# Kernel tuning notes

Measured on AMD Instinct MI355X. Metric: run time of the kernel, lower is better.

The kernel has to match this reference:

```python
import jax, jax.numpy as jnp
import numpy as np

NUM_HEADS = 8
D_MODEL = 512
D_K = D_MODEL // NUM_HEADS


def setup_inputs() -> dict:
    key = jax.random.key(0)
    ks = jax.random.split(key, 16)
    B, L, Dq = 4, 2048, 512
    s = 1.0 / np.sqrt(D_MODEL)
    inp = {
        "query": jax.random.normal(ks[0], (B, L, Dq), jnp.float32),
        "key": jax.random.normal(ks[1], (B, L, Dq), jnp.float32),
        "value": jax.random.normal(ks[2], (B, L, Dq), jnp.float32),
        "mask": jax.random.randint(ks[3], (B, L), 0, 2, jnp.int32),
        "Wq": jax.random.normal(ks[4], (Dq, D_MODEL), jnp.float32) * s,
        "bq": jax.random.normal(ks[5], (D_MODEL,), jnp.float32) * s,
        "Wk": jax.random.normal(ks[6], (Dq, D_MODEL), jnp.float32) * s,
        "bk": jax.random.normal(ks[7], (D_MODEL,), jnp.float32) * s,
        "Wv": jax.random.normal(ks[8], (Dq, D_MODEL), jnp.float32) * s,
        "bv": jax.random.normal(ks[9], (D_MODEL,), jnp.float32) * s,
        "Wo": jax.random.normal(ks[10], (D_MODEL, D_MODEL), jnp.float32) * s,
        "bo": jax.random.normal(ks[11], (D_MODEL,), jnp.float32) * s,
    }
    return inp


def _mha(query, key, value, mask, Wq, bq, Wk, bk, Wv, bv, Wo, bo):
    B, Q, _ = query.shape
    KV = key.shape[1]
    # projections, split into heads: (B, H, L, d_k)
    q = (query @ Wq + bq).reshape(B, Q, NUM_HEADS, D_K).transpose(0, 2, 1, 3)
    k = (key @ Wk + bk).reshape(B, KV, NUM_HEADS, D_K).transpose(0, 2, 1, 3)
    v = (value @ Wv + bv).reshape(B, KV, NUM_HEADS, D_K).transpose(0, 2, 1, 3)
    # full (B, H, Q, KV) score matrix, as in the original module
    scores = jnp.einsum("bhqd,bhkd->bhqk", q, k) / jnp.sqrt(jnp.asarray(D_K, q.dtype))
    m = (mask == 0)[:, None, None, :]  # (B,1,1,KV) broadcasting like unsqueeze(1)
    min_val = jnp.finfo(scores.dtype).min
    scores = jnp.where(m, min_val, scores)
    attn = jax.nn.softmax(scores, axis=-1)
    attn = jnp.where(m, 0.0, attn)
    xs = jnp.einsum("bhqk,bhkd->bhqd", attn, v)
    xs = xs.transpose(0, 2, 1, 3).reshape(B, Q, NUM_HEADS * D_K)
    return xs @ Wo + bo


def reference(query, key, value, mask, Wq, bq, Wk, bk, Wv, bv, Wo, bo):
    return _mha(query, key, value, mask, Wq, bq, Wk, bk, Wv, bv, Wo, bo)
```

## Files before the change

### kernel.cpp

```cpp
#include <hip/hip_runtime.h>
#include <math.h>

#define Bq 4
#define Lq 2048
#define NH 8
#define LDP6 36

typedef __attribute__((ext_vector_type(8))) __bf16 bf16x8;
typedef __attribute__((ext_vector_type(4))) float f32x4;
#define MFMA16(a,b,c) __builtin_amdgcn_mfma_f32_16x16x32_bf16(a,b,c,0,0,0)

__device__ __forceinline__ void async16(const void* g, void* l) {
    __builtin_amdgcn_global_load_lds(
        (const __attribute__((address_space(1))) unsigned int*)g,
        (__attribute__((address_space(3))) unsigned int*)l, 16, 0, 0);
}

__device__ __forceinline__ void splitbf(float x, ushort& h, ushort& l) {
    unsigned u = __float_as_uint(x);
    h = (ushort)(u >> 16);
    float hf = __uint_as_float(u & 0xffff0000u);
    l = (ushort)(__float_as_uint(x - hf) >> 16);
}
__device__ __forceinline__ ushort rnebf(float x) {
    unsigned u = __float_as_uint(x);
    return (ushort)((u + 0x7fffu + ((u >> 16) & 1u)) >> 16);
}

__global__ __launch_bounds__(256) void maskscan_kernel(
    const int* __restrict__ mask, int* __restrict__ idx, int* __restrict__ nvalid)
{
    __shared__ int ss[256];
    const int b = blockIdx.x, tid = threadIdx.x;
    int m[8], s = 0;
    #pragma unroll
    for (int j = 0; j < 8; ++j) { m[j] = (mask[b * 2048 + tid * 8 + j] != 0); s += m[j]; }
    int v = s;
    ss[tid] = v;
    __syncthreads();
    for (int off = 1; off < 256; off <<= 1) {
        int t_ = (tid >= off) ? ss[tid - off] : 0;
        __syncthreads();
        v += t_;
        ss[tid] = v;
        __syncthreads();
    }
    int pos = v - s;
    #pragma unroll
    for (int j = 0; j < 8; ++j) if (m[j]) idx[b * 2048 + pos++] = tid * 8 + j;
    int tot = ss[255];
    if (tid == 0) nvalid[b] = tot;
    for (int k = tot + tid; k < 2048; k += 256) idx[b * 2048 + k] = 0;
}

__global__ __launch_bounds__(256) void xrne3_kernel(
    const float* __restrict__ X0, const float* __restrict__ X1, const float* __restrict__ X2,
    const int* __restrict__ idx, const int* __restrict__ nvalid,
    ushort* __restrict__ Xr)
{
    const int z = blockIdx.z;
    const float* X = (z == 0) ? X0 : (z == 1) ? X1 : X2;
    const size_t ebase = (size_t)blockIdx.x * 2048 + (size_t)threadIdx.x * 8;
    const int row = (int)(ebase >> 9), col = (int)(ebase & 511);
    const int b = row >> 11, r = row & 2047;
    if (z >= 1) {
        int nv = nvalid[b];
        int nvpad = ((nv + 127) >> 7) << 7;
        if (r >= nvpad) return;
    }
    const int srow = (z == 0) ? row : (b * 2048 + idx[b * 2048 + r]);
    const float* src = X + (size_t)srow * 512 + col;
    float4 a = *(const float4*)(src);
    float4 bb = *(const float4*)(src + 4);
    float vv[8] = {a.x, a.y, a.z, a.w, bb.x, bb.y, bb.z, bb.w};
    ushort hs[8];
    #pragma unroll
    for (int j = 0; j < 8; ++j) hs[j] = rnebf(vv[j]);
    uint4 wh;
    wh.x = hs[0] | ((unsigned)hs[1] << 16); wh.y = hs[2] | ((unsigned)hs[3] << 16);
    wh.z = hs[4] | ((unsigned)hs[5] << 16); wh.w = hs[6] | ((unsigned)hs[7] << 16);
    *(uint4*)(Xr + (size_t)z * 8192 * 512 + ebase) = wh;
}

__global__ __launch_bounds__(256) void wsplit4_kernel(
    const float* __restrict__ W0, const float* __restrict__ W1,
    const float* __restrict__ W2, const float* __restrict__ W3,
    ushort* __restrict__ WTh, ushort* __restrict__ WTl)
{
    __shared__ float T[64][65];
    const int z = blockIdx.z;
    const float* W = (z == 0) ? W0 : (z == 1) ? W1 : (z == 2) ? W2 : W3;
    const int k0 = blockIdx.x * 64, n0 = blockIdx.y * 64;
    const int tid = threadIdx.x;
    #pragma unroll
    for (int i = 0; i < 4; ++i) {
        int u = tid + i * 256;
        int row = u >> 4, c4 = (u & 15) * 4;
        float4 v = *(const float4*)(W + (size_t)(k0 + row) * 512 + n0 + c4);
        T[row][c4 + 0] = v.x; T[row][c4 + 1] = v.y; T[row][c4 + 2] = v.z; T[row][c4 + 3] = v.w;
    }
    __syncthreads();
    #pragma unroll
    for (int i = 0; i < 2; ++i) {
        int u = tid + i * 256;
        int d = u >> 3, c8 = (u & 7) * 8;
        ushort hs[8], ls[8];
        #pragma unroll
        for (int j = 0; j < 8; ++j) splitbf(T[c8 + j][d], hs[j], ls[j]);
        uint4 wh, wl;
        wh.x = hs[0] | ((unsigned)hs[1] << 16); wh.y = hs[2] | ((unsigned)hs[3] << 16);
        wh.z = hs[4] | ((unsigned)hs[5] << 16); wh.w = hs[6] | ((unsigned)hs[7] << 16);
        wl.x = ls[0] | ((unsigned)ls[1] << 16); wl.y = ls[2] | ((unsigned)ls[3] << 16);
        wl.z = ls[4] | ((unsigned)ls[5] << 16); wl.w = ls[6] | ((unsigned)ls[7] << 16);
        size_t off = (size_t)(z * 512 + n0 + d) * 512 + k0 + c8;
        *(uint4*)(WTh + off) = wh;
        *(uint4*)(WTl + off) = wl;
    }
}

union GS {
    struct {
        ushort A[2][4096];
        ushort Bh[2][4096];
        ushort Bl[2][4096];
    } s;
    ushort E[24576];
};

__global__ __launch_bounds__(256) void gemm2_kernel(
    const ushort* __restrict__ Ap,
    const ushort* __restrict__ BhT, const ushort* __restrict__ BlT,
    const float* __restrict__ b0, const float* __restrict__ b1, const float* __restrict__ b2,
    const int* __restrict__ nvalid, int final_, float* __restrict__ Cf,
    ushort* __restrict__ Qh, ushort* __restrict__ Khp, ushort* __restrict__ VhT)
{
    __shared__ __align__(16) GS gs;
    const int tid = threadIdx.x;
    const int wave = tid >> 6, lane = tid & 63;
    const int l15 = lane & 15, quad = lane >> 4;
    const int m0 = blockIdx.x * 128;
    const int yy = blockIdx.y;
    const int mi = yy >> 2, n0 = (yy & 3) * 128;
    const int nglob = mi * 512 + n0;

    if (!final_ && mi >= 1) {
        int nv = nvalid[m0 >> 11];
        int nvpad = ((nv + 127) >> 7) << 7;
        if ((m0 & 2047) >= nvpad) return;
    }

    const float* bias = (mi == 0) ? b0 : (mi == 1) ? b1 : b2;
    const int wm = (wave & 1) * 64, wn = (wave >> 1) * 64;

    const ushort* AZ = Ap + (size_t)mi * 8192 * 512;
    const int arow = lane >> 2;
    const int acs = ((lane & 3) ^ ((arow >> 1) & 3)) * 8;
    const ushort* asrc[2]; int adst[2];
    #pragma unroll
    for (int j = 0; j < 2; ++j) {
        int rb = wave * 2 + j;
        asrc[j] = AZ + (size_t)(m0 + rb * 16 + arow) * 512 + acs;
        adst[j] = rb * 512 + lane * 8;
    }
    const int brow = lane >> 2;
    const int bcs = ((lane & 3) ^ (brow & 3)) * 8;
    const ushort* bsh[2]; const ushort* bsl[2]; int bdst[2];
    #pragma unroll
    for (int j = 0; j < 2; ++j) {
        int r2 = wave * 32 + j * 16 + brow;
        bsh[j] = BhT + (size_t)(nglob + r2) * 512 + bcs;
        bsl[j] = BlT + (size_t)(nglob + r2) * 512 + bcs;
        bdst[j] = wave * 1024 + j * 512 + lane * 8;
    }

    f32x4 acc[4][4];
    #pragma unroll
    for (int i = 0; i < 4; ++i)
        #pragma unroll
        for (int j = 0; j < 4; ++j) acc[i][j] = (f32x4){0.f, 0.f, 0.f, 0.f};

    #pragma unroll
    for (int j = 0; j < 2; ++j) {
        async16(asrc[j], &gs.s.A[0][adst[j]]);
        async16(bsh[j], &gs.s.Bh[0][bdst[j]]);
        async16(bsl[j], &gs.s.Bl[0][bdst[j]]);
    }

    for (int t = 0; t < 16; ++t) {
        const int p = t & 1;
        __syncthreads();
        if (t < 15) {
            const int kn = (t + 1) * 32;
            #pragma unroll
            for (int j = 0; j < 2; ++j) {
                async16(asrc[j] + kn, &gs.s.A[1 - p][adst[j]]);
                async16(bsh[j] + kn, &gs.s.Bh[1 - p][bdst[j]]);
                async16(bsl[j] + kn, &gs.s.Bl[1 - p][bdst[j]]);
            }
        }
        bf16x8 af[4];
        #pragma unroll
        for (int ms = 0; ms < 4; ++ms) {
            int off = (wm + ms * 16 + l15) * 32 + (quad ^ ((l15 >> 1) & 3)) * 8;
            af[ms] = *(const bf16x8*)&gs.s.A[p][off];
        }
        #pragma unroll
        for (int ns = 0; ns < 4; ++ns) {
            int off = (wn + ns * 16 + l15) * 32 + (quad ^ (l15 & 3)) * 8;
            bf16x8 bfh = *(const bf16x8*)&gs.s.Bh[p][off];
            bf16x8 bfl = *(const bf16x8*)&gs.s.Bl[p][off];
            #pragma unroll
            for (int ms = 0; ms < 4; ++ms) {
                acc[ms][ns] = MFMA16(af[ms], bfl, acc[ms][ns]);
                acc[ms][ns] = MFMA16(af[ms], bfh, acc[ms][ns]);
            }
        }
    }

    #pragma unroll
    for (int ns = 0; ns < 4; ++ns) {
        float bv = bias[n0 + wn + ns * 16 + l15];
        #pragma unroll
        for (int ms = 0; ms < 4; ++ms)
            #pragma unroll
            for (int r = 0; r < 4; ++r) acc[ms][ns][r] += bv;
    }

    if (final_) {
        #pragma unroll
        for (int ns = 0; ns < 4; ++ns) {
            int col = n0 + wn + ns * 16 + l15;
            #pragma unroll
            for (int ms = 0; ms < 4; ++ms)
                #pragma unroll
                for (int r = 0; r < 4; ++r)
                    Cf[(size_t)(m0 + wm + ms * 16 + quad * 4 + r) * 512 + col] = acc[ms][ns][r];
        }
        return;
    }

    const int h0 = n0 >> 6;
    const int b = m0 >> 11, rr0 = m0 & 2047;
    __syncthreads();
    #pragma unroll
    for (int ms = 0; ms < 4; ++ms) {
        #pragma unroll
        for (int ns = 0; ns < 4; ++ns) {
            int cl = wn + ns * 16 + l15;
            int rl = wm + ms * 16 + quad * 4;
            if (mi == 2) {
                ushort4 w4;
                #pragma unroll
                for (int r = 0; r < 4; ++r) ((ushort*)&w4)[r] = rnebf(acc[ms][ns][r]);
                *(ushort4*)&gs.E[cl * 136 + rl] = w4;
            } else {
                #pragma unroll
                for (int r = 0; r < 4; ++r) gs.E[(rl + r) * 136 + cl] = rnebf(acc[ms][ns][r]);
            }
        }
    }
    __syncthreads();
    if (mi == 2) {
        #pragma unroll
        for (int i = 0; i < 8; ++i) {
            int idx2 = tid + i * 256;
            int d = idx2 >> 4, rg = idx2 & 15;
            int head = d >> 6, dd = d & 63;
            uint4 u = *(const uint4*)&gs.E[d * 136 + rg * 8];
            *(uint4*)&VhT[((size_t)(b * 8 + h0 + head) * 64 + dd) * 2048 + rr0 + rg * 8] = u;
        }
    } else {
        ushort* dst = (mi == 0) ? Qh : Khp;
        #pragma unroll
        for (int i = 0; i < 8; ++i) {
            int idx2 = tid + i * 256;
            int row = idx2 >> 4, cg = idx2 & 15;
            int head = cg >> 3, c8 = (cg & 7) * 8;
            uint4 u = *(const uint4*)&gs.E[row * 136 + cg * 8];
            *(uint4*)&dst[((size_t)(b * 8 + h0 + head) * 2048 + rr0 + row) * 64 + c8] = u;
        }
    }
}

union SmemU {
    struct { ushort KVs[2][4][4096]; ushort Pp[8][64 * LDP6]; } p1;
    struct { float Obuf[4][64 * 68]; float Lbuf[4][64]; } p2;
};

__global__ __launch_bounds__(512, 2) void attn3_kernel(
    const ushort* __restrict__ Qh, const ushort* __restrict__ Kh,
    const ushort* __restrict__ VhT, const int* __restrict__ nvalid,
    ushort* __restrict__ XS)
{
    __shared__ SmemU smem;
    const int tid = threadIdx.x;
    const int wave = tid >> 6, lane = tid & 63;
    const int l15 = lane & 15, quad = lane >> 4;
    const int w4 = wave & 3, half = wave >> 2;
    const int bh = blockIdx.x, b = bh >> 3, h = bh & 7;
    const int q0 = blockIdx.y * 256;

    const int nv = nvalid[b];
    const int nt = (nv + 127) >> 7;
    const int kvofs = half * 64 * nt;

    bf16x8 qf[4][2];
    #pragma unroll
    for (int qs = 0; qs < 4; ++qs) {
        size_t qb = ((size_t)bh * 2048 + q0 + w4 * 64 + qs * 16 + l15) * 64 + quad * 8;
        qf[qs][0] = *(const bf16x8*)(Qh + qb);
        qf[qs][1] = *(const bf16x8*)(Qh + qb + 32);
    }

    const f32x4 z = {0.f, 0.f, 0.f, 0.f};
    f32x4 oacc[4][4];
    #pragma unroll
    for (int i = 0; i < 4; ++i)
        #pragma unroll
        for (int j = 0; j < 4; ++j) oacc[i][j] = z;
    float lacc[4] = {0.f, 0.f, 0.f, 0.f};

    const int rloc = lane >> 3, gsw = (lane & 7) ^ rloc;
    const ushort* sb[4]; size_t sstep[4]; int dofs[4];
    #pragma unroll
    for (int i = 0; i < 4; ++i) {
        int cc = wave * 4 + i;
        int hc = cc >> 4, r16 = cc & 15, pc = r16 >> 3, ic = r16 & 7;
        if (pc == 0) {
            sb[i] = Kh + ((size_t)(bh * 2048 + hc * 64 * nt + ic * 8 + rloc)) * 64 + gsw * 8;
            sstep[i] = (size_t)64 * 64;
        } else {
            sb[i] = VhT + ((size_t)(bh * 64 + ic * 8 + rloc)) * 2048 + hc * 64 * nt + gsw * 8;
            sstep[i] = 64;
        }
        dofs[i] = (hc * 2 + pc) * 4096 + ic * 512;
    }

    const int sw0 = (quad ^ (l15 & 7)) * 8;
    const float SCL = 0.18033688011112042f;

    if (nt > 0) {
        #pragma unroll
        for (int i = 0; i < 4; ++i)
            async16(sb[i], &smem.p1.KVs[0][0][0] + dofs[i]);
    }

    for (int t = 0; t < nt; ++t) {
        __syncthreads();
        if (t + 1 < nt) {
            #pragma unroll
            for (int i = 0; i < 4; ++i)
                async16(sb[i] + (size_t)(t + 1) * sstep[i], &smem.p1.KVs[(t + 1) & 1][0][0] + dofs[i]);
        }
        const int p = t & 1;
        const ushort* K0 = smem.p1.KVs[p][half * 2 + 0];
        const ushort* V0 = smem.p1.KVs[p][half * 2 + 1];
        ushort* Pw = smem.p1.Pp[wave];

        #pragma unroll
        for (int ks = 0; ks < 2; ++ks) {
            #pragma unroll
            for (int kt2 = 0; kt2 < 2; ++kt2) {
                const int kt = ks * 2 + kt2;
                const int kb = (kt * 16 + l15) * 64;
                bf16x8 ka0 = *(const bf16x8*)&K0[kb + sw0];
                bf16x8 ka1 = *(const bf16x8*)&K0[kb + (sw0 ^ 32)];
                const int kbase = kvofs + t * 64 + kt * 16 + quad * 4;
                float bias[4];
                #pragma unroll
                for (int r = 0; r < 4; ++r) bias[r] = (kbase + r < nv) ? 0.f : -1e38f;
                #pragma unroll
                for (int qs = 0; qs < 4; ++qs) {
                    f32x4 a = z;
                    a = MFMA16(ka0, qf[qs][0], a);
                    a = MFMA16(ka1, qf[qs][1], a);
                    float pv[4];
                    #pragma unroll
                    for (int r = 0; r < 4; ++r) {
                        float x = __builtin_fmaf(a[r], SCL, bias[r]);
                        float e; asm("v_exp_f32 %0, %1" : "=v"(e) : "v"(x));
                        lacc[qs] += e;
                        pv[r] = e;
                    }
                    unsigned u01, u23;
                    asm("v_cvt_pk_bf16_f32 %0, %1, %2" : "=v"(u01) : "v"(pv[0]), "v"(pv[1]));
                    asm("v_cvt_pk_bf16_f32 %0, %1, %2" : "=v"(u23) : "v"(pv[2]), "v"(pv[3]));
                    uint2 w2; w2.x = u01; w2.y = u23;
                    *(uint2*)&Pw[(qs * 16 + l15) * LDP6 + kt2 * 16 + quad * 4] = w2;
                }
            }
            const int svo = sw0 ^ (ks * 32);
            bf16x8 pf[4];
            #pragma unroll
            for (int qs = 0; qs < 4; ++qs)
                pf[qs] = *(const bf16x8*)&Pw[(qs * 16 + l15) * LDP6 + quad * 8];
            #pragma unroll
            for (int dsub = 0; dsub < 4; ++dsub) {
                const int vb = (dsub * 16 + l15) * 64;
                bf16x8 vh = *(const bf16x8*)&V0[vb + svo];
                #pragma unroll
                for (int qs = 0; qs < 4; ++qs)
                    oacc[qs][dsub] = MFMA16(vh, pf[qs], oacc[qs][dsub]);
            }
        }
    }

    float lv[4];
    #pragma unroll
    for (int qs = 0; qs < 4; ++qs) {
        float v = lacc[qs];
        v += __shfl_xor(v, 16);
        v += __shfl_xor(v, 32);
        lv[qs] = v;
    }

    __syncthreads();
    if (half == 1) {
        #pragma unroll
        for (int qs = 0; qs < 4; ++qs) {
            #pragma unroll
            for (int dsub = 0; dsub < 4; ++dsub) {
                float4 o4 = {oacc[qs][dsub][0], oacc[qs][dsub][1], oacc[qs][dsub][2], oacc[qs][dsub][3]};
                *(float4*)&smem.p2.Obuf[w4][(qs * 16 + l15) * 68 + dsub * 16 + quad * 4] = o4;
            }
            if (quad == 0) smem.p2.Lbuf[w4][qs * 16 + l15] = lv[qs];
        }
    }
    __syncthreads();
    if (half == 0) {
        #pragma unroll
        for (int qs = 0; qs < 4; ++qs) {
            float ltot = lv[qs] + smem.p2.Lbuf[w4][qs * 16 + l15];
            float inv = (ltot > 0.f) ? 1.f / ltot : 0.f;
            int row = q0 + w4 * 64 + qs * 16 + l15;
            ushort* rp = XS + ((size_t)(b * 2048 + row)) * 512 + h * 64;
            #pragma unroll
            for (int dsub = 0; dsub < 4; ++dsub) {
                float4 p4 = *(const float4*)&smem.p2.Obuf[w4][(qs * 16 + l15) * 68 + dsub * 16 + quad * 4];
                ushort4 hv;
                hv.x = rnebf((oacc[qs][dsub][0] + p4.x) * inv);
                hv.y = rnebf((oacc[qs][dsub][1] + p4.y) * inv);
                hv.z = rnebf((oacc[qs][dsub][2] + p4.z) * inv);
                hv.w = rnebf((oacc[qs][dsub][3] + p4.w) * inv);
                *(ushort4*)&rp[dsub * 16 + quad * 4] = hv;
            }
        }
    }
}

extern "C" void kernel_launch(void* const* d_in, const int* in_sizes, int n_in,
                              void* d_out, int out_size, void* d_ws, size_t ws_size,
                              hipStream_t stream) {
    const float* query = (const float*)d_in[0];
    const float* key   = (const float*)d_in[1];
    const float* value = (const float*)d_in[2];
    const int*   mask  = (const int*)d_in[3];
    const float* Wq = (const float*)d_in[4];
    const float* bq = (const float*)d_in[5];
    const float* Wk = (const float*)d_in[6];
    const float* bk = (const float*)d_in[7];
    const float* Wv = (const float*)d_in[8];
    const float* bv = (const float*)d_in[9];
    const float* Wo = (const float*)d_in[10];
    const float* bo = (const float*)d_in[11];

    char* w = (char*)d_ws;
    const size_t MB = (size_t)1 << 20;
    ushort* Qh  = (ushort*)(w + 0 * MB);
    ushort* XS  = (ushort*)(w + 8 * MB);
    ushort* Khp = (ushort*)(w + 16 * MB);
    ushort* VhT = (ushort*)(w + 24 * MB);
    ushort* Xr  = (ushort*)(w + 32 * MB);
    ushort* WTh = (ushort*)(w + 80 * MB);
    ushort* WTl = (ushort*)(w + 82 * MB);
    int* idxbuf = (int*)(w + 84 * MB);
    int* nvbuf  = (int*)(w + 84 * MB + 65536);

    maskscan_kernel<<<dim3(4), 256, 0, stream>>>(mask, idxbuf, nvbuf);
    xrne3_kernel<<<dim3(2048, 1, 3), 256, 0, stream>>>(query, key, value, idxbuf, nvbuf, Xr);
    wsplit4_kernel<<<dim3(8, 8, 4), 256, 0, stream>>>(Wq, Wk, Wv, Wo, WTh, WTl);
    gemm2_kernel<<<dim3(64, 12), 256, 0, stream>>>(
        Xr, WTh, WTl, bq, bk, bv, nvbuf, 0, nullptr, Qh, Khp, VhT);
    attn3_kernel<<<dim3(32, 8), 512, 0, stream>>>(Qh, Khp, VhT, nvbuf, XS);
    gemm2_kernel<<<dim3(64, 4), 256, 0, stream>>>(
        XS, WTh + (size_t)1536 * 512, WTl + (size_t)1536 * 512,
        bo, bo, bo, nvbuf, 1, (float*)d_out,
        nullptr, nullptr, nullptr);
}
```

Measured before the change: 203.7 us.

## Fuse fp32-to-bf16 input conversion and gather into QKV GEMM loads; merge prep kernels

New measurement: 208.1 us. 2.2% more time.

```diff
diff --git a/kernel.cpp b/kernel.cpp
--- a/kernel.cpp
+++ b/kernel.cpp
@@ -27,71 +27,42 @@
     return (ushort)((u + 0x7fffu + ((u >> 16) & 1u)) >> 16);
 }
 
-__global__ __launch_bounds__(256) void maskscan_kernel(
+__global__ __launch_bounds__(256) void prep_kernel(
+    const float* __restrict__ W0, const float* __restrict__ W1,
+    const float* __restrict__ W2, const float* __restrict__ W3,
+    ushort* __restrict__ WTh, ushort* __restrict__ WTl,
     const int* __restrict__ mask, int* __restrict__ idx, int* __restrict__ nvalid)
 {
-    __shared__ int ss[256];
-    const int b = blockIdx.x, tid = threadIdx.x;
-    int m[8], s = 0;
-    #pragma unroll
-    for (int j = 0; j < 8; ++j) { m[j] = (mask[b * 2048 + tid * 8 + j] != 0); s += m[j]; }
-    int v = s;
-    ss[tid] = v;
-    __syncthreads();
-    for (int off = 1; off < 256; off <<= 1) {
-        int t_ = (tid >= off) ? ss[tid - off] : 0;
-        __syncthreads();
-        v += t_;
+    const int tid = threadIdx.x;
+    if (blockIdx.z == 4) {
+        if (blockIdx.x >= 4 || blockIdx.y != 0) return;
+        __shared__ int ss[256];
+        const int b = blockIdx.x;
+        int m[8], s = 0;
+        #pragma unroll
+        for (int j = 0; j < 8; ++j) { m[j] = (mask[b * 2048 + tid * 8 + j] != 0); s += m[j]; }
+        int v = s;
         ss[tid] = v;
         __syncthreads();
-    }
-    int pos = v - s;
-    #pragma unroll
-    for (int j = 0; j < 8; ++j) if (m[j]) idx[b * 2048 + pos++] = tid * 8 + j;
-    int tot = ss[255];
-    if (tid == 0) nvalid[b] = tot;
-    for (int k = tot + tid; k < 2048; k += 256) idx[b * 2048 + k] = 0;
-}
-
-__global__ __launch_bounds__(256) void xrne3_kernel(
-    const float* __restrict__ X0, const float* __restrict__ X1, const float* __restrict__ X2,
-    const int* __restrict__ idx, const int* __restrict__ nvalid,
-    ushort* __restrict__ Xr)
-{
-    const int z = blockIdx.z;
-    const float* X = (z == 0) ? X0 : (z == 1) ? X1 : X2;
-    const size_t ebase = (size_t)blockIdx.x * 2048 + (size_t)threadIdx.x * 8;
-    const int row = (int)(ebase >> 9), col = (int)(ebase & 511);
-    const int b = row >> 11, r = row & 2047;
-    if (z >= 1) {
-        int nv = nvalid[b];
-        int nvpad = ((nv + 127) >> 7) << 7;
-        if (r >= nvpad) return;
-    }
-    const int srow = (z == 0) ? row : (b * 2048 + idx[b * 2048 + r]);
-    const float* src = X + (size_t)srow * 512 + col;
-    float4 a = *(const float4*)(src);
-    float4 bb = *(const float4*)(src + 4);
-    float vv[8] = {a.x, a.y, a.z, a.w, bb.x, bb.y, bb.z, bb.w};
-    ushort hs[8];
-    #pragma unroll
-    for (int j = 0; j < 8; ++j) hs[j] = rnebf(vv[j]);
-    uint4 wh;
-    wh.x = hs[0] | ((unsigned)hs[1] << 16); wh.y = hs[2] | ((unsigned)hs[3] << 16);
-    wh.z = hs[4] | ((unsigned)hs[5] << 16); wh.w = hs[6] | ((unsigned)hs[7] << 16);
-    *(uint4*)(Xr + (size_t)z * 8192 * 512 + ebase) = wh;
-}
-
-__global__ __launch_bounds__(256) void wsplit4_kernel(
-    const float* __restrict__ W0, const float* __restrict__ W1,
-    const float* __restrict__ W2, const float* __restrict__ W3,
-    ushort* __restrict__ WTh, ushort* __restrict__ WTl)
-{
+        for (int off = 1; off < 256; off <<= 1) {
+            int t_ = (tid >= off) ? ss[tid - off] : 0;
+            __syncthreads();
+            v += t_;
+            ss[tid] = v;
+            __syncthreads();
+        }
+        int pos = v - s;
+        #pragma unroll
+        for (int j = 0; j < 8; ++j) if (m[j]) idx[b * 2048 + pos++] = tid * 8 + j;
+        int tot = ss[255];
+        if (tid == 0) nvalid[b] = tot;
+        for (int k = tot + tid; k < 2048; k += 256) idx[b * 2048 + k] = 0;
+        return;
+    }
     __shared__ float T[64][65];
     const int z = blockIdx.z;
     const float* W = (z == 0) ? W0 : (z == 1) ? W1 : (z == 2) ? W2 : W3;
     const int k0 = blockIdx.x * 64, n0 = blockIdx.y * 64;
-    const int tid = threadIdx.x;
     #pragma unroll
     for (int i = 0; i < 4; ++i) {
         int u = tid + i * 256;
@@ -127,11 +98,11 @@
     ushort E[24576];
 };
 
-__global__ __launch_bounds__(256) void gemm2_kernel(
-    const ushort* __restrict__ Ap,
+__global__ __launch_bounds__(256) void gemmqkv_kernel(
+    const float* __restrict__ Xq, const float* __restrict__ Xk, const float* __restrict__ Xv,
+    const int* __restrict__ idx, const int* __restrict__ nvalid,
     const ushort* __restrict__ BhT, const ushort* __restrict__ BlT,
     const float* __restrict__ b0, const float* __restrict__ b1, const float* __restrict__ b2,
-    const int* __restrict__ nvalid, int final_, float* __restrict__ Cf,
     ushort* __restrict__ Qh, ushort* __restrict__ Khp, ushort* __restrict__ VhT)
 {
     __shared__ __align__(16) GS gs;
@@ -142,25 +113,29 @@
     const int yy = blockIdx.y;
     const int mi = yy >> 2, n0 = (yy & 3) * 128;
     const int nglob = mi * 512 + n0;
-
-    if (!final_ && mi >= 1) {
-        int nv = nvalid[m0 >> 11];
+    const int b = m0 >> 11;
+
+    if (mi >= 1) {
+        int nv = nvalid[b];
         int nvpad = ((nv + 127) >> 7) << 7;
         if ((m0 & 2047) >= nvpad) return;
     }
 
+    const float* X = (mi == 0) ? Xq : (mi == 1) ? Xk : Xv;
     const float* bias = (mi == 0) ? b0 : (mi == 1) ? b1 : b2;
     const int wm = (wave & 1) * 64, wn = (wave >> 1) * 64;
 
-    const ushort* AZ = Ap + (size_t)mi * 8192 * 512;
-    const int arow = lane >> 2;
-    const int acs = ((lane & 3) ^ ((arow >> 1) & 3)) * 8;
-    const ushort* asrc[2]; int adst[2];
-    #pragma unroll
-    for (int j = 0; j < 2; ++j) {
-        int rb = wave * 2 + j;
-        asrc[j] = AZ + (size_t)(m0 + rb * 16 + arow) * 512 + acs;
-        adst[j] = rb * 512 + lane * 8;
+    const int am = tid >> 3, ak = (tid & 7) * 4;
+    const float* asrc[4]; int adst[4];
+    #pragma unroll
+    for (int i = 0; i < 4; ++i) {
+        int row = am + 32 * i;
+        int grow = m0 + row, r = grow & 2047;
+        int srow = (mi == 0) ? grow : (b * 2048 + idx[b * 2048 + r]);
+        asrc[i] = X + (size_t)srow * 512 + ak;
+        int c = (tid & 7) >> 1;
+        int cp = c ^ ((row >> 1) & 3);
+        adst[i] = row * 32 + cp * 8 + (tid & 1) * 4;
     }
     const int brow = lane >> 2;
     const int bcs = ((lane & 3) ^ (brow & 3)) * 8;
@@ -179,11 +154,20 @@
         #pragma unroll
         for (int j = 0; j < 4; ++j) acc[i][j] = (f32x4){0.f, 0.f, 0.f, 0.f};
 
+    float4 av[4];
+    #pragma unroll
+    for (int i = 0; i < 4; ++i) av[i] = *(const float4*)(asrc[i]);
     #pragma unroll
     for (int j = 0; j < 2; ++j) {
-        async16(asrc[j], &gs.s.A[0][adst[j]]);
         async16(bsh[j], &gs.s.Bh[0][bdst[j]]);
         async16(bsl[j], &gs.s.Bl[0][bdst[j]]);
+    }
+    #pragma unroll
+    for (int i = 0; i < 4; ++i) {
+        ushort4 h4;
+        h4.x = rnebf(av[i].x); h4.y = rnebf(av[i].y);
+        h4.z = rnebf(av[i].z); h4.w = rnebf(av[i].w);
+        *(ushort4*)&gs.s.A[0][adst[i]] = h4;
     }
 
     for (int t = 0; t < 16; ++t) {
@@ -193,10 +177,11 @@
             const int kn = (t + 1) * 32;
             #pragma unroll
             for (int j = 0; j < 2; ++j) {
-                async16(asrc[j] + kn, &gs.s.A[1 - p][adst[j]]);
                 async16(bsh[j] + kn, &gs.s.Bh[1 - p][bdst[j]]);
                 async16(bsl[j] + kn, &gs.s.Bl[1 - p][bdst[j]]);
             }
+            #pragma unroll
+            for (int i = 0; i < 4; ++i) av[i] = *(const float4*)(asrc[i] + kn);
         }
         bf16x8 af[4];
         #pragma unroll
@@ -215,6 +200,15 @@
                 acc[ms][ns] = MFMA16(af[ms], bfh, acc[ms][ns]);
             }
         }
+        if (t < 15) {
+            #pragma unroll
+            for (int i = 0; i < 4; ++i) {
+                ushort4 h4;
+                h4.x = rnebf(av[i].x); h4.y = rnebf(av[i].y);
+                h4.z = rnebf(av[i].z); h4.w = rnebf(av[i].w);
+                *(ushort4*)&gs.s.A[1 - p][adst[i]] = h4;
+            }
+        }
     }
 
     #pragma unroll
@@ -226,21 +220,8 @@
             for (int r = 0; r < 4; ++r) acc[ms][ns][r] += bv;
     }
 
-    if (final_) {
-        #pragma unroll
-        for (int ns = 0; ns < 4; ++ns) {
-            int col = n0 + wn + ns * 16 + l15;
-            #pragma unroll
-            for (int ms = 0; ms < 4; ++ms)
-                #pragma unroll
-                for (int r = 0; r < 4; ++r)
-                    Cf[(size_t)(m0 + wm + ms * 16 + quad * 4 + r) * 512 + col] = acc[ms][ns][r];
-        }
-        return;
-    }
-
     const int h0 = n0 >> 6;
-    const int b = m0 >> 11, rr0 = m0 & 2047;
+    const int rr0 = m0 & 2047;
     __syncthreads();
     #pragma unroll
     for (int ms = 0; ms < 4; ++ms) {
@@ -278,6 +259,96 @@
             int head = cg >> 3, c8 = (cg & 7) * 8;
             uint4 u = *(const uint4*)&gs.E[row * 136 + cg * 8];
             *(uint4*)&dst[((size_t)(b * 8 + h0 + head) * 2048 + rr0 + row) * 64 + c8] = u;
+        }
+    }
+}
+
+__global__ __launch_bounds__(256) void gemmo_kernel(
+    const ushort* __restrict__ Ap,
+    const ushort* __restrict__ BhT, const ushort* __restrict__ BlT,
+    const float* __restrict__ bias, float* __restrict__ Cf)
+{
+    __shared__ __align__(16) GS gs;
+    const int tid = threadIdx.x;
+    const int wave = tid >> 6, lane = tid & 63;
+    const int l15 = lane & 15, quad = lane >> 4;
+    const int m0 = blockIdx.x * 128;
+    const int n0 = blockIdx.y * 128;
+    const int wm = (wave & 1) * 64, wn = (wave >> 1) * 64;
+
+    const int arow = lane >> 2;
+    const int acs = ((lane & 3) ^ ((arow >> 1) & 3)) * 8;
+    const ushort* asrc[2]; int adst[2];
+    #pragma unroll
+    for (int j = 0; j < 2; ++j) {
+        int rb = wave * 2 + j;
+        asrc[j] = Ap + (size_t)(m0 + rb * 16 + arow) * 512 + acs;
+        adst[j] = rb * 512 + lane * 8;
+    }
+    const int brow = lane >> 2;
+    const int bcs = ((lane & 3) ^ (brow & 3)) * 8;
+    const ushort* bsh[2]; const ushort* bsl[2]; int bdst[2];
+    #pragma unroll
+    for (int j = 0; j < 2; ++j) {
+        int r2 = wave * 32 + j * 16 + brow;
+        bsh[j] = BhT + (size_t)(n0 + r2) * 512 + bcs;
+        bsl[j] = BlT + (size_t)(n0 + r2) * 512 + bcs;
+        bdst[j] = wave * 1024 + j * 512 + lane * 8;
+    }
+
+    f32x4 acc[4][4];
+    #pragma unroll
+    for (int i = 0; i < 4; ++i)
+        #pragma unroll
+        for (int j = 0; j < 4; ++j) acc[i][j] = (f32x4){0.f, 0.f, 0.f, 0.f};
+
+    #pragma unroll
+    for (int j = 0; j < 2; ++j) {
+        async16(asrc[j], &gs.s.A[0][adst[j]]);
+        async16(bsh[j], &gs.s.Bh[0][bdst[j]]);
+        async16(bsl[j], &gs.s.Bl[0][bdst[j]]);
+    }
+
+    for (int t = 0; t < 16; ++t) {
+        const int p = t & 1;
+        __syncthreads();
+        if (t < 15) {
+            const int kn = (t + 1) * 32;
+            #pragma unroll
+            for (int j = 0; j < 2; ++j) {
+                async16(asrc[j] + kn, &gs.s.A[1 - p][adst[j]]);
+                async16(bsh[j] + kn, &gs.s.Bh[1 - p][bdst[j]]);
+                async16(bsl[j] + kn, &gs.s.Bl[1 - p][bdst[j]]);
+            }
+        }
+        bf16x8 af[4];
+        #pragma unroll
+        for (int ms = 0; ms < 4; ++ms) {
+            int off = (wm + ms * 16 + l15) * 32 + (quad ^ ((l15 >> 1) & 3)) * 8;
+            af[ms] = *(const bf16x8*)&gs.s.A[p][off];
+        }
+        #pragma unroll
+        for (int ns = 0; ns < 4; ++ns) {
+            int off = (wn + ns * 16 + l15) * 32 + (quad ^ (l15 & 3)) * 8;
+            bf16x8 bfh = *(const bf16x8*)&gs.s.Bh[p][off];
+            bf16x8 bfl = *(const bf16x8*)&gs.s.Bl[p][off];
+            #pragma unroll
+            for (int ms = 0; ms < 4; ++ms) {
+                acc[ms][ns] = MFMA16(af[ms], bfl, acc[ms][ns]);
+                acc[ms][ns] = MFMA16(af[ms], bfh, acc[ms][ns]);
+            }
+        }
+    }
+
+    #pragma unroll
+    for (int ns = 0; ns < 4; ++ns) {
+        float bv = bias[n0 + wn + ns * 16 + l15];
+        #pragma unroll
+        for (int ms = 0; ms < 4; ++ms) {
+            int col = n0 + wn + ns * 16 + l15;
+            #pragma unroll
+            for (int r = 0; r < 4; ++r)
+                Cf[(size_t)(m0 + wm + ms * 16 + quad * 4 + r) * 512 + col] = acc[ms][ns][r] + bv;
         }
     }
 }
@@ -470,20 +541,16 @@
     ushort* XS  = (ushort*)(w + 8 * MB);
     ushort* Khp = (ushort*)(w + 16 * MB);
     ushort* VhT = (ushort*)(w + 24 * MB);
-    ushort* Xr  = (ushort*)(w + 32 * MB);
-    ushort* WTh = (ushort*)(w + 80 * MB);
-    ushort* WTl = (ushort*)(w + 82 * MB);
-    int* idxbuf = (int*)(w + 84 * MB);
-    int* nvbuf  = (int*)(w + 84 * MB + 65536);
-
-    maskscan_kernel<<<dim3(4), 256, 0, stream>>>(mask, idxbuf, nvbuf);
-    xrne3_kernel<<<dim3(2048, 1, 3), 256, 0, stream>>>(query, key, value, idxbuf, nvbuf, Xr);
-    wsplit4_kernel<<<dim3(8, 8, 4), 256, 0, stream>>>(Wq, Wk, Wv, Wo, WTh, WTl);
-    gemm2_kernel<<<dim3(64, 12), 256, 0, stream>>>(
-        Xr, WTh, WTl, bq, bk, bv, nvbuf, 0, nullptr, Qh, Khp, VhT);
+    ushort* WTh = (ushort*)(w + 32 * MB);
+    ushort* WTl = (ushort*)(w + 34 * MB);
+    int* idxbuf = (int*)(w + 36 * MB);
+    int* nvbuf  = (int*)(w + 36 * MB + 65536);
+
+    prep_kernel<<<dim3(8, 8, 5), 256, 0, stream>>>(
+        Wq, Wk, Wv, Wo, WTh, WTl, mask, idxbuf, nvbuf);
+    gemmqkv_kernel<<<dim3(64, 12), 256, 0, stream>>>(
+        query, key, value, idxbuf, nvbuf, WTh, WTl, bq, bk, bv, Qh, Khp, VhT);
     attn3_kernel<<<dim3(32, 8), 512, 0, stream>>>(Qh, Khp, VhT, nvbuf, XS);
-    gemm2_kernel<<<dim3(64, 4), 256, 0, stream>>>(
-        XS, WTh + (size_t)1536 * 512, WTl + (size_t)1536 * 512,
-        bo, bo, bo, nvbuf, 1, (float*)d_out,
-        nullptr, nullptr, nullptr);
-}
+    gemmo_kernel<<<dim3(64, 4), 256, 0, stream>>>(
+        XS, WTh + (size_t)1536 * 512, WTl + (size_t)1536 * 512, bo, (float*)d_out);
+}
```
